# Kernel tuning notes

Measured on AMD Instinct MI355X. Metric: run time of the kernel, lower is better.

The kernel has to match this reference:

```python
import jax, jax.numpy as jnp
import numpy as np

B, T, H, V = 4, 512, 2048, 32000
BETA = 0.1          # KL coefficient vs reference model
EPS_LOW = 0.2       # PPO clip lower
EPS_HIGH = 0.2      # PPO clip upper
TEMP = 1.0          # logit temperature


def _per_token_logps(h, w, ids):
    # h: [B,T,H], w: [V,H], ids: [B,T] -> log p(token_id) per position
    logits = jnp.einsum('bth,vh->btv', h, w) / TEMP          # [B,T,V]
    logps = jax.nn.log_softmax(logits.astype(jnp.float32), axis=-1)
    return jnp.take_along_axis(logps, ids[..., None], axis=-1)[..., 0]  # [B,T]


def setup_inputs() -> dict:
    key = jax.random.key(0)
    k = jax.random.split(key, 6)
    x = jax.random.normal(k[0], (B, T, H), jnp.float32)
    ref_input = jax.random.normal(k[1], (B, T, H), jnp.float32)
    lin_weight = jax.random.normal(k[2], (V, H), jnp.float32) * (H ** -0.5)
    ref_weight = jax.random.normal(k[3], (V, H), jnp.float32) * (H ** -0.5)
    selected_token_ids = jax.random.randint(k[4], (B, T), 0, V)
    attention_mask = jnp.ones((B, T), jnp.int32)
    advantages = jax.random.normal(k[5], (B,), jnp.float32)
    return {
        'x': x,
        'lin_weight': lin_weight,
        'ref_input': ref_input,
        'ref_weight': ref_weight,
        'advantages': advantages,
        'selected_token_ids': selected_token_ids,
        'attention_mask': attention_mask,
    }


def reference(x, lin_weight, ref_input, ref_weight, advantages,
              selected_token_ids, attention_mask):
    # policy per-token log-probs (fused linear + log-softmax + gather)
    logps = _per_token_logps(x, lin_weight, selected_token_ids)            # [B,T]
    # reference model path runs under no_grad in the original
    ref_logps = jax.lax.stop_gradient(
        _per_token_logps(ref_input, ref_weight, selected_token_ids))      # [B,T]
    # old_per_token_logps=None -> detached current logps (ratio==1 in fwd)
    old_logps = jax.lax.stop_gradient(logps)

    coef1 = jnp.exp(logps - old_logps)
    coef2 = jnp.clip(coef1, 1.0 - EPS_LOW, 1.0 + EPS_HIGH)
    adv = advantages[:, None]                                             # [B,1]
    per_token_loss = -jnp.minimum(coef1 * adv, coef2 * adv)

    # KL(ref || policy) surrogate: exp(d) - d - 1 with d = ref - cur
    d = ref_logps - logps
    kl = jnp.exp(d) - d - 1.0
    per_token_loss = per_token_loss + BETA * kl

    mask = attention_mask.astype(jnp.float32)
    # loss_type='bnpo': global masked token mean
    loss = jnp.sum(per_token_loss * mask) / jnp.maximum(jnp.sum(mask), 1.0)
    return loss
```

## Files before the change

### kernel.cpp

```cpp
#include <hip/hip_runtime.h>
#include <hip/hip_bf16.h>

#define B_ 4
#define T_ 512
#define H_ 2048
#define V_ 32000
#define M_ (B_ * T_)
#define BETA_ 0.1f

#define BM 256
#define BN 256
#define BK 64
#define NKT (H_ / BK)
#define NTILES (V_ / BN)
#define NP (NTILES * 4)
#define NPAD 512
#define GRID_GEMM 1024

#define ABYTES (BM * BK * 2)
#define BUFBYTES (2 * ABYTES)
#define LDS_TOTAL (2 * BUFBYTES)

typedef __attribute__((ext_vector_type(8))) short short8;
typedef __attribute__((ext_vector_type(4))) float f32x4;

__device__ __forceinline__ void async_copy16(const void* g, void* l) {
  __builtin_amdgcn_global_load_lds(
      (const __attribute__((address_space(1))) void*)g,
      (__attribute__((address_space(3))) void*)l, 16, 0, 0);
}

__device__ __forceinline__ unsigned short f2bf(float f) {
  unsigned int u = __float_as_uint(f);
  u += 0x7fffu + ((u >> 16) & 1u);
  return (unsigned short)(u >> 16);
}

__global__ void cvt_bf16_kernel(const float* __restrict__ in,
                                unsigned short* __restrict__ out, int n4) {
  int i = blockIdx.x * blockDim.x + threadIdx.x;
  if (i < n4) {
    float4 v = ((const float4*)in)[i];
    ushort4 o;
    o.x = f2bf(v.x); o.y = f2bf(v.y); o.z = f2bf(v.z); o.w = f2bf(v.w);
    ((ushort4*)out)[i] = o;
  }
}

__global__ void sel_kernel(const float* __restrict__ x, const float* __restrict__ w,
                           const float* __restrict__ rx, const float* __restrict__ rw,
                           const int* __restrict__ ids, float* __restrict__ sel) {
  int gw = (blockIdx.x * 256 + threadIdx.x) >> 6;
  int l = threadIdx.x & 63;
  int md = gw >> 11;
  int m = gw & (M_ - 1);
  const float* xr = (md ? rx : x) + (size_t)m * H_;
  const float* wr = (md ? rw : w) + (size_t)ids[m] * H_;
  float s = 0.0f;
#pragma unroll
  for (int it = 0; it < H_ / 256; ++it) {
    int k = it * 256 + l * 4;
    float4 a = *(const float4*)(xr + k);
    float4 b = *(const float4*)(wr + k);
    s += a.x * b.x + a.y * b.y + a.z * b.z + a.w * b.w;
  }
#pragma unroll
  for (int off = 32; off; off >>= 1) s += __shfl_xor(s, off, 64);
  if (l == 0) sel[md * M_ + m] = s;
}

__global__ __launch_bounds__(512, 2) void gemm_lse_kernel(
    const unsigned short* __restrict__ A,
    const unsigned short* __restrict__ Bw,
    float* __restrict__ pmax,
    float* __restrict__ psum) {
  const int linear = blockIdx.x;
  const int c = linear & 7, g = linear >> 3;
  const int nt = (g >> 3) * 8 + c;
  if (nt >= NTILES) return;
  const int mb = g & 7;

  extern __shared__ char smem[];

  const int tid = threadIdx.x;
  const int w = tid >> 6, l = tid & 63;
  const int quad = l >> 4, lr = l & 15;
  const int wr = w >> 2, wc = w & 3;
  const int m0 = mb * BM, n0 = nt * BN;

  const int srow = tid & 255, shi = tid >> 8;
  const unsigned short* gA = A + (size_t)(m0 + srow) * H_ + shi * 8;
  const unsigned short* gB = Bw + (size_t)(n0 + srow) * H_ + shi * 8;
  const int ldsoff = (shi * 256 + srow) * 16;

  f32x4 acc[8][4] = {};

  const int abOff = quad * 4096 + (wr * 128 + lr) * 16;
  const int bbOff = ABYTES + quad * 4096 + (wc * 64 + lr) * 16;

  auto stage = [&](int p, int kt) {
    const unsigned short* a = gA + kt * BK;
    const unsigned short* b = gB + kt * BK;
    char* la = smem + p * BUFBYTES + ldsoff;
    char* lb = la + ABYTES;
#pragma unroll
    for (int j = 0; j < 4; ++j) {
      async_copy16(a + j * 16, la + j * 8192);
      async_copy16(b + j * 16, lb + j * 8192);
    }
  };

  auto compute = [&](int p) {
    const char* ab = smem + p * BUFBYTES + abOff;
    const char* bb = smem + p * BUFBYTES + bbOff;
#pragma unroll
    for (int kk = 0; kk < 2; ++kk) {
      short8 af[8], bf[4];
#pragma unroll
      for (int i = 0; i < 8; ++i)
        af[i] = *(const short8*)(ab + kk * 16384 + i * 256);
#pragma unroll
      for (int j = 0; j < 4; ++j)
        bf[j] = *(const short8*)(bb + kk * 16384 + j * 256);
      __builtin_amdgcn_s_setprio(1);
#pragma unroll
      for (int i = 0; i < 8; ++i)
#pragma unroll
        for (int j = 0; j < 4; ++j)
          acc[i][j] = __builtin_amdgcn_mfma_f32_16x16x32_bf16(
              af[i], bf[j], acc[i][j], 0, 0, 0);
      __builtin_amdgcn_s_setprio(0);
    }
  };

  stage(0, 0);
  __syncthreads();
  int p = 0;
  for (int kt = 1; kt < NKT; ++kt) {
    stage(p ^ 1, kt);
    compute(p);
    __syncthreads();
    p ^= 1;
  }
  compute(p);

  const int p_idx = nt * 4 + wc;
#pragma unroll
  for (int i = 0; i < 8; ++i) {
#pragma unroll
    for (int r = 0; r < 4; ++r) {
      float vmax = fmaxf(fmaxf(acc[i][0][r], acc[i][1][r]),
                         fmaxf(acc[i][2][r], acc[i][3][r]));
#pragma unroll
      for (int off = 8; off; off >>= 1) vmax = fmaxf(vmax, __shfl_xor(vmax, off, 64));
      float s = __expf(acc[i][0][r] - vmax) + __expf(acc[i][1][r] - vmax) +
                __expf(acc[i][2][r] - vmax) + __expf(acc[i][3][r] - vmax);
#pragma unroll
      for (int off = 8; off; off >>= 1) s += __shfl_xor(s, off, 64);
      if (lr == 0) {
        int mg = m0 + wr * 128 + i * 16 + quad * 4 + r;
        pmax[(size_t)mg * NPAD + p_idx] = vmax;
        psum[(size_t)mg * NPAD + p_idx] = s;
      }
    }
  }
}

__global__ void lse_merge_kernel(
    const float* __restrict__ pmaxP, const float* __restrict__ psumP,
    const float* __restrict__ pmaxR, const float* __restrict__ psumR,
    const float* __restrict__ sel, float* __restrict__ lp) {
  int gw = (blockIdx.x * 256 + threadIdx.x) >> 6;
  int l = threadIdx.x & 63;
  int md = gw >> 11, m = gw & (M_ - 1);
  const float* pm = (md ? pmaxR : pmaxP) + (size_t)m * NPAD;
  const float* ps = (md ? psumR : psumP) + (size_t)m * NPAD;
  float mx = -3.0e38f, s = 0.0f;
  for (int p = l; p < NP; p += 64) {
    float a = pm[p], b = ps[p];
    float nm = fmaxf(mx, a);
    s = s * __expf(mx - nm) + b * __expf(a - nm);
    mx = nm;
  }
#pragma unroll
  for (int off = 32; off; off >>= 1) {
    float omx = __shfl_xor(mx, off, 64);
    float os  = __shfl_xor(s, off, 64);
    float nm = fmaxf(mx, omx);
    s = s * __expf(mx - nm) + os * __expf(omx - nm);
    mx = nm;
  }
  if (l == 0) lp[md * M_ + m] = sel[md * M_ + m] - (mx + __logf(s));
}

__global__ void loss_kernel(const float* __restrict__ lp,
                            const float* __restrict__ adv,
                            const int* __restrict__ mask,
                            float* __restrict__ out) {
  __shared__ float sp[16], sm[16];
  int t = threadIdx.x;
  float pt = 0.0f, mk = 0.0f;
  for (int m = t; m < M_; m += 1024) {
    float d = lp[M_ + m] - lp[m];
    float kl = __expf(d) - d - 1.0f;
    float mkm = (float)mask[m];
    pt += (-adv[m >> 9] + BETA_ * kl) * mkm;
    mk += mkm;
  }
#pragma unroll
  for (int off = 32; off; off >>= 1) {
    pt += __shfl_xor(pt, off, 64);
    mk += __shfl_xor(mk, off, 64);
  }
  int wv = t >> 6, l = t & 63;
  if (l == 0) { sp[wv] = pt; sm[wv] = mk; }
  __syncthreads();
  if (t == 0) {
    float a = 0.0f, b = 0.0f;
#pragma unroll
    for (int i = 0; i < 16; ++i) { a += sp[i]; b += sm[i]; }
    out[0] = a / fmaxf(b, 1.0f);
  }
}

extern "C" void kernel_launch(void* const* d_in, const int* in_sizes, int n_in,
                              void* d_out, int out_size, void* d_ws, size_t ws_size,
                              hipStream_t stream) {
  const float* x    = (const float*)d_in[0];
  const float* lw   = (const float*)d_in[1];
  const float* rx   = (const float*)d_in[2];
  const float* rw   = (const float*)d_in[3];
  const float* adv  = (const float*)d_in[4];
  const int*   ids  = (const int*)d_in[5];
  const int*   mask = (const int*)d_in[6];
  float* out = (float*)d_out;

  static bool s_attr_set = false;
  if (!s_attr_set) {
    hipFuncSetAttribute(reinterpret_cast<const void*>(gemm_lse_kernel),
                        hipFuncAttributeMaxDynamicSharedMemorySize, LDS_TOTAL);
    s_attr_set = true;
  }

  char* ws = (char*)d_ws;
  unsigned short* Wb = (unsigned short*)ws;
  unsigned short* xb = (unsigned short*)(ws + (size_t)V_ * H_ * 2);
  char* p0 = ws + (size_t)V_ * H_ * 2 + (size_t)M_ * H_ * 2;
  const size_t PSZ = (size_t)M_ * NPAD * 4;
  float* pmaxP = (float*)(p0);
  float* psumP = (float*)(p0 + 1 * PSZ);
  float* pmaxR = (float*)(p0 + 2 * PSZ);
  float* psumR = (float*)(p0 + 3 * PSZ);
  float* sel   = (float*)(p0 + 4 * PSZ);
  float* lp    = (float*)(p0 + 4 * PSZ + 2 * M_ * 4);

  const int n4x = M_ * H_ / 4, n4w = V_ * H_ / 4;

  cvt_bf16_kernel<<<(n4x + 255) / 256, 256, 0, stream>>>(x, xb, n4x);
  cvt_bf16_kernel<<<(n4w + 255) / 256, 256, 0, stream>>>(lw, Wb, n4w);
  sel_kernel<<<(2 * M_) / 4, 256, 0, stream>>>(x, lw, rx, rw, ids, sel);
  gemm_lse_kernel<<<GRID_GEMM, 512, LDS_TOTAL, stream>>>(xb, Wb, pmaxP, psumP);
  cvt_bf16_kernel<<<(n4x + 255) / 256, 256, 0, stream>>>(rx, xb, n4x);
  cvt_bf16_kernel<<<(n4w + 255) / 256, 256, 0, stream>>>(rw, Wb, n4w);
  gemm_lse_kernel<<<GRID_GEMM, 512, LDS_TOTAL, stream>>>(xb, Wb, pmaxR, psumR);

  lse_merge_kernel<<<(2 * M_) / 4, 256, 0, stream>>>(pmaxP, psumP, pmaxR, psumR,
                                                     sel, lp);
  loss_kernel<<<1, 1024, 0, stream>>>(lp, adv, mask, out);
}
```

Measured before the change: 1.689 ms.

## Switch GEMM mainloop to triple-buffered BK=32 pipeline with explicit vmcnt waits

Halves the K-tile size and moves from double to triple buffering in LDS, issuing loads two stages ahead. It uses explicit s_waitcnt vmcnt counts and raw s_barrier instead of __syncthreads, so the wait only covers the oldest outstanding stage. The aim is to keep more global loads in flight and overlap them with MFMA work. In exchange it adds twice as many barriers per K step, and correctness now depends on the hand-counted vmcnt values.

Result: faster. 1.431 ms (-15.3%).

```diff
diff --git a/kernel.cpp b/kernel.cpp
--- a/kernel.cpp
+++ b/kernel.cpp
@@ -10,16 +10,17 @@
 
 #define BM 256
 #define BN 256
-#define BK 64
+#define BK 32
 #define NKT (H_ / BK)
 #define NTILES (V_ / BN)
 #define NP (NTILES * 4)
 #define NPAD 512
 #define GRID_GEMM 1024
 
-#define ABYTES (BM * BK * 2)
-#define BUFBYTES (2 * ABYTES)
-#define LDS_TOTAL (2 * BUFBYTES)
+#define TILEB (BM * BK * 2)
+#define BUFB (2 * TILEB)
+#define NBUF 3
+#define LDS_TOTAL (NBUF * BUFB)
 
 typedef __attribute__((ext_vector_type(8))) short short8;
 typedef __attribute__((ext_vector_type(4))) float f32x4;
@@ -28,6 +29,14 @@
   __builtin_amdgcn_global_load_lds(
       (const __attribute__((address_space(1))) void*)g,
       (__attribute__((address_space(3))) void*)l, 16, 0, 0);
+}
+
+__device__ __forceinline__ void hard_barrier() {
+  asm volatile("" ::: "memory");
+  __builtin_amdgcn_sched_barrier(0);
+  __builtin_amdgcn_s_barrier();
+  __builtin_amdgcn_sched_barrier(0);
+  asm volatile("" ::: "memory");
 }
 
 __device__ __forceinline__ unsigned short f2bf(float f) {
@@ -91,58 +100,57 @@
   const int srow = tid & 255, shi = tid >> 8;
   const unsigned short* gA = A + (size_t)(m0 + srow) * H_ + shi * 8;
   const unsigned short* gB = Bw + (size_t)(n0 + srow) * H_ + shi * 8;
-  const int ldsoff = (shi * 256 + srow) * 16;
 
   f32x4 acc[8][4] = {};
 
   const int abOff = quad * 4096 + (wr * 128 + lr) * 16;
-  const int bbOff = ABYTES + quad * 4096 + (wc * 64 + lr) * 16;
-
-  auto stage = [&](int p, int kt) {
+  const int bbOff = TILEB + quad * 4096 + (wc * 64 + lr) * 16;
+
+  auto stage = [&](int b, int kt) {
     const unsigned short* a = gA + kt * BK;
-    const unsigned short* b = gB + kt * BK;
-    char* la = smem + p * BUFBYTES + ldsoff;
-    char* lb = la + ABYTES;
-#pragma unroll
-    for (int j = 0; j < 4; ++j) {
-      async_copy16(a + j * 16, la + j * 8192);
-      async_copy16(b + j * 16, lb + j * 8192);
-    }
+    const unsigned short* bsrc = gB + kt * BK;
+    char* la = smem + b * BUFB + tid * 16;
+    char* lb = la + TILEB;
+    async_copy16(a, la);
+    async_copy16(a + 16, la + 8192);
+    async_copy16(bsrc, lb);
+    async_copy16(bsrc + 16, lb + 8192);
   };
 
-  auto compute = [&](int p) {
-    const char* ab = smem + p * BUFBYTES + abOff;
-    const char* bb = smem + p * BUFBYTES + bbOff;
-#pragma unroll
-    for (int kk = 0; kk < 2; ++kk) {
-      short8 af[8], bf[4];
-#pragma unroll
-      for (int i = 0; i < 8; ++i)
-        af[i] = *(const short8*)(ab + kk * 16384 + i * 256);
+  auto compute = [&](int b) {
+    const char* ab = smem + b * BUFB + abOff;
+    const char* bb = smem + b * BUFB + bbOff;
+    short8 af[8], bf[4];
+#pragma unroll
+    for (int i = 0; i < 8; ++i) af[i] = *(const short8*)(ab + i * 256);
+#pragma unroll
+    for (int j = 0; j < 4; ++j) bf[j] = *(const short8*)(bb + j * 256);
+    __builtin_amdgcn_s_setprio(1);
+#pragma unroll
+    for (int i = 0; i < 8; ++i)
 #pragma unroll
       for (int j = 0; j < 4; ++j)
-        bf[j] = *(const short8*)(bb + kk * 16384 + j * 256);
-      __builtin_amdgcn_s_setprio(1);
-#pragma unroll
-      for (int i = 0; i < 8; ++i)
-#pragma unroll
-        for (int j = 0; j < 4; ++j)
-          acc[i][j] = __builtin_amdgcn_mfma_f32_16x16x32_bf16(
-              af[i], bf[j], acc[i][j], 0, 0, 0);
-      __builtin_amdgcn_s_setprio(0);
-    }
+        acc[i][j] = __builtin_amdgcn_mfma_f32_16x16x32_bf16(
+            af[i], bf[j], acc[i][j], 0, 0, 0);
+    __builtin_amdgcn_s_setprio(0);
   };
 
   stage(0, 0);
-  __syncthreads();
-  int p = 0;
-  for (int kt = 1; kt < NKT; ++kt) {
-    stage(p ^ 1, kt);
-    compute(p);
-    __syncthreads();
-    p ^= 1;
-  }
-  compute(p);
+  stage(1, 1);
+  for (int t = 0; t < NKT - 2; ++t) {
+    stage((t + 2) % NBUF, t + 2);
+    asm volatile("s_waitcnt vmcnt(8)" ::: "memory");
+    hard_barrier();
+    compute(t % NBUF);
+    hard_barrier();
+  }
+  asm volatile("s_waitcnt vmcnt(4)" ::: "memory");
+  hard_barrier();
+  compute((NKT - 2) % NBUF);
+  hard_barrier();
+  asm volatile("s_waitcnt vmcnt(0)" ::: "memory");
+  hard_barrier();
+  compute((NKT - 1) % NBUF);
 
   const int p_idx = nt * 4 + wc;
 #pragma unroll
```
